# Kernel tuning notes

Hardware: AMD Instinct MI355X
Metric: run time of the kernel (lower is better)

## Reference

```python
import jax, jax.numpy as jnp
import numpy as np

B, S, F, K = 64, 1024, 128, 64  # batch, seq(=l), feat(=d), bottleneck k


def setup_inputs() -> dict:
    key = jax.random.key(0)
    ks = jax.random.split(key, 24)
    r = lambda k_, sh, s=0.05: (jax.random.normal(k_, sh, dtype=jnp.float32) * s)
    inp = {
        'f1_norm': jax.random.normal(ks[0], (B, S, F), dtype=jnp.float32),
        'f2_norm': jax.random.normal(ks[1], (B, S, F), dtype=jnp.float32),
        'f3_norm': jax.random.normal(ks[2], (B, S, F), dtype=jnp.float32),
        # AMLP params (Linear(F, 2F))
        'Wi': r(ks[3], (2 * F, F)), 'bi': r(ks[4], (2 * F,)),
        'Wq': r(ks[5], (2 * F, F)), 'bq': r(ks[6], (2 * F,)),
        'Wvp': r(ks[7], (2 * F, F)), 'bvp': r(ks[8], (2 * F,)),
        # affine_{a,v,l}: Linear(l, l, bias=False) -> weight [l, l]
        'Aa': r(ks[9], (S, S)), 'Av': r(ks[10], (S, S)), 'Al': r(ks[11], (S, S)),
        # W_{a,v,t}: Linear(l, k) -> [k, l]
        'Wa': r(ks[12], (K, S)), 'Wv': r(ks[13], (K, S)), 'Wt': r(ks[14], (K, S)),
        # W_c{a,v,t}: Linear(2d, k) -> [k, 2F]
        'Wca': r(ks[15], (K, 2 * F)), 'Wcv': r(ks[16], (K, 2 * F)), 'Wct': r(ks[17], (K, 2 * F)),
        # W_h{a,v,t}: Linear(k, l) -> [l, k]
        'Wha': r(ks[18], (S, K)), 'Whv': r(ks[19], (S, K)), 'Wht': r(ks[20], (S, K)),
    }
    return inp


def _amlp(txt, aud, vis, Wi, bi, Wq, bq, Wvp, bvp):
    f1 = jnp.einsum('bsf,gf->bsg', txt, Wi) + bi  # [B,S,2F]
    f2 = jnp.einsum('bsf,gf->bsg', aud, Wq) + bq
    f3 = jnp.einsum('bsf,gf->bsg', vis, Wvp) + bvp
    n1 = jnp.linalg.norm(f1)
    n2 = jnp.linalg.norm(f2)
    n3 = jnp.linalg.norm(f3)
    # faithful to source: third term is scalar factor3 * norm3 (broadcast)
    exp_out = (n1 / (n1 + n2)) * f1 + (n2 / (n1 + n2)) * f2 + (n3 / (n1 + n2 + n3)) * n3
    b, s, g = exp_out.shape
    z = exp_out.reshape(b, s, g // 2, 2).sum(-1)  # AvgPool1d(2,2) * 2 == pair sum
    # F.normalize default dim=1 (over sequence axis for 3D tensor)
    z = z / jnp.maximum(jnp.linalg.norm(z, axis=1, keepdims=True), 1e-12)
    return z  # [B,S,F]


def reference(f1_norm, f2_norm, f3_norm, Wi, bi, Wq, bq, Wvp, bvp,
              Aa, Av, Al, Wa, Wv, Wt, Wca, Wcv, Wct, Wha, Whv, Wht):
    txt, aud, vis = f1_norm, f2_norm, f3_norm
    G = _amlp(txt, aud, vis, Wi, bi, Wq, bq, Wvp, bvp)  # [B,S,F]

    G_ag = jnp.concatenate([aud, G], axis=-1)  # [B,S,2F]
    G_vg = jnp.concatenate([vis, G], axis=-1)
    G_lg = jnp.concatenate([txt, G], axis=-1)
    scale = np.sqrt(G_ag.shape[-1]).astype(np.float32)  # sqrt(2F); same for all three

    # a_j = affine(G_xg^T); att = x^T @ a_j^T  ==  x^T @ (A @ G_xg)
    AGa = jnp.einsum('ts,bsc->btc', Aa, G_ag)
    C_a = jnp.tanh(jnp.einsum('bsf,bsc->bfc', aud, AGa) / scale)  # [B,F,2F]
    AGv = jnp.einsum('ts,bsc->btc', Av, G_ag)  # NOTE: source bug uses G_ag, not G_vg
    C_v = jnp.tanh(jnp.einsum('bsf,bsc->bfc', vis, AGv) / scale)
    AGl = jnp.einsum('ts,bsc->btc', Al, G_lg)
    C_t = jnp.tanh(jnp.einsum('bsf,bsc->bfc', txt, AGl) / scale)

    H_a = jax.nn.relu(jnp.einsum('bfc,kc->bfk', C_a, Wca) + jnp.einsum('bsf,ks->bfk', aud, Wa))
    H_v = jax.nn.relu(jnp.einsum('bfc,kc->bfk', C_v, Wcv) + jnp.einsum('bsf,ks->bfk', vis, Wv))
    H_t = jax.nn.relu(jnp.einsum('bfc,kc->bfk', C_t, Wct) + jnp.einsum('bsf,ks->bfk', txt, Wt))

    out_a = jnp.einsum('bfk,sk->bsf', H_a, Wha) + aud  # [B,S,F]
    out_v = jnp.einsum('bfk,sk->bsf', H_v, Whv) + vis
    out_t = jnp.einsum('bfk,sk->bsf', H_t, Wht) + txt
    return (out_t, out_a, out_v)
```

## Files before the change

kernel.cpp:

```cpp
#include <hip/hip_runtime.h>
#include <math.h>

constexpr int Bb = 64;
constexpr int Ss = 1024;
constexpr int Ff = 128;
constexpr int G2 = 256;
constexpr int Kk = 64;
constexpr int NA = 1024;

typedef __bf16 bfrag __attribute__((ext_vector_type(8)));
typedef float  facc  __attribute__((ext_vector_type(4)));
typedef short  s8v   __attribute__((ext_vector_type(8)));
typedef short  s4v   __attribute__((ext_vector_type(4)));

__device__ __forceinline__ short f2bfs(float f) {
  union { float f; unsigned u; } v; v.f = f;
  unsigned r = v.u + 0x7FFFu + ((v.u >> 16) & 1u);
  return (short)(r >> 16);
}
__device__ __forceinline__ float bf2fs(short s) {
  union { unsigned u; float f; } v; v.u = ((unsigned)(unsigned short)s) << 16;
  return v.f;
}
__device__ __forceinline__ facc mfma16(bfrag a, bfrag b, facc c) {
  return __builtin_amdgcn_mfma_f32_16x16x32_bf16(a, b, c, 0, 0, 0);
}
__device__ __forceinline__ void gld16(const void* g, void* l) {
  __builtin_amdgcn_global_load_lds(
      (const __attribute__((address_space(1))) void*)g,
      (__attribute__((address_space(3))) void*)l, 16, 0, 0);
}

__global__ void k_transpose(const float* __restrict__ aud, const float* __restrict__ vis,
                            const float* __restrict__ txt, short* __restrict__ xT) {
  __shared__ float tile[64][65];
  int z = blockIdx.z;
  int mod = z >> 6, b = z & 63;
  const float* x = (mod == 0) ? aud : (mod == 1) ? vis : txt;
  int s0 = blockIdx.x * 64, f0 = blockIdx.y * 64;
  int tid = threadIdx.x;
  {
    int fg = tid & 15, sb = tid >> 4;
#pragma unroll
    for (int i = 0; i < 4; ++i) {
      int si = i * 16 + sb;
      float4 v = *(const float4*)(x + ((size_t)b * Ss + s0 + si) * Ff + f0 + fg * 4);
      tile[si][fg * 4 + 0] = v.x;
      tile[si][fg * 4 + 1] = v.y;
      tile[si][fg * 4 + 2] = v.z;
      tile[si][fg * 4 + 3] = v.w;
    }
  }
  __syncthreads();
  short* dst = xT + ((size_t)mod * Bb + b) * Ff * Ss;
  {
    int sg = tid & 15, fb = tid >> 4;
#pragma unroll
    for (int i = 0; i < 4; ++i) {
      int fi = i * 16 + fb;
      s4v v;
      v[0] = f2bfs(tile[sg * 4 + 0][fi]);
      v[1] = f2bfs(tile[sg * 4 + 1][fi]);
      v[2] = f2bfs(tile[sg * 4 + 2][fi]);
      v[3] = f2bfs(tile[sg * 4 + 3][fi]);
      *(s4v*)(dst + (size_t)(f0 + fi) * Ss + s0 + sg * 4) = v;
    }
  }
}

__global__ void k_build_aextT(const float* __restrict__ Aa, const float* __restrict__ Av,
                              const float* __restrict__ Al, short* __restrict__ aextT) {
  __shared__ float tile[64][65];
  int mod = blockIdx.z;
  const float* A = (mod == 0) ? Aa : (mod == 1) ? Av : Al;
  short* dst = aextT + (size_t)mod * NA * Ss;
  int n0 = blockIdx.x * 64, t0 = blockIdx.y * 64;
  int tid = threadIdx.x;
  {
    int fg = tid & 15, sb = tid >> 4;
#pragma unroll
    for (int i = 0; i < 4; ++i) {
      int ti = i * 16 + sb;
      float4 v = *(const float4*)(A + (size_t)(t0 + ti) * Ss + n0 + fg * 4);
      tile[ti][fg * 4 + 0] = v.x;
      tile[ti][fg * 4 + 1] = v.y;
      tile[ti][fg * 4 + 2] = v.z;
      tile[ti][fg * 4 + 3] = v.w;
    }
  }
  __syncthreads();
  {
    int tg = tid & 15, nb = tid >> 4;
#pragma unroll
    for (int i = 0; i < 4; ++i) {
      int nj = i * 16 + nb;
      s4v v;
      v[0] = f2bfs(tile[tg * 4 + 0][nj]);
      v[1] = f2bfs(tile[tg * 4 + 1][nj]);
      v[2] = f2bfs(tile[tg * 4 + 2][nj]);
      v[3] = f2bfs(tile[tg * 4 + 3][nj]);
      *(s4v*)(dst + (size_t)(n0 + nj) * Ss + t0 + tg * 4) = v;
    }
  }
}

__global__ void k_build_w(const float* __restrict__ Wca, const float* __restrict__ Wcv,
                          const float* __restrict__ Wct, const float* __restrict__ Wha,
                          const float* __restrict__ Whv, const float* __restrict__ Wht,
                          const float* __restrict__ Wi, const float* __restrict__ Wq,
                          const float* __restrict__ Wvp, const float* __restrict__ Wa,
                          const float* __restrict__ Wv, const float* __restrict__ Wt,
                          short* __restrict__ wcb, short* __restrict__ whb,
                          short* __restrict__ wbar, short* __restrict__ wsb) {
  int idx = blockIdx.x * 256 + threadIdx.x;
  const int n1 = 3 * Kk * G2;
  const int n2 = n1 + 3 * Ss * Kk;
  const int n3 = n2 + 3 * G2 * Ff;
  if (idx < n1) {
    int mod = idx / (Kk * G2), r = idx - mod * (Kk * G2);
    const float* W = (mod == 0) ? Wca : (mod == 1) ? Wcv : Wct;
    wcb[idx] = f2bfs(W[r]);
  } else if (idx < n2) {
    int j = idx - n1;
    int mod = j / (Ss * Kk), r = j - mod * (Ss * Kk);
    const float* W = (mod == 0) ? Wha : (mod == 1) ? Whv : Wht;
    whb[j] = f2bfs(W[r]);
  } else if (idx < n3) {
    int j = idx - n2;
    int mod = j / (G2 * Ff), r = j - mod * (G2 * Ff);
    int n = r >> 7, k = r & 127;
    int t = n >> 4, nl = n & 15;
    int c = k >> 5, q = (k >> 3) & 3, e = k & 7;
    const float* W = (mod == 0) ? Wi : (mod == 1) ? Wq : Wvp;
    wbar[mod * G2 * Ff + (((t * 4 + c) * 64 + q * 16 + nl) * 8) + e] = f2bfs(W[r]);
  } else {
    int j = idx - n3;
    int mod = j / (Kk * Ss), r = j - mod * (Kk * Ss);
    const float* W = (mod == 0) ? Wa : (mod == 1) ? Wv : Wt;
    wsb[j] = f2bfs(W[r]);
  }
}

__global__ void __launch_bounds__(256, 3) k_amlp(
    const float* __restrict__ txt, const float* __restrict__ aud, const float* __restrict__ vis,
    const float* __restrict__ bi, const float* __restrict__ bq, const float* __restrict__ bvp,
    const short* __restrict__ wbar,
    short* __restrict__ p1, short* __restrict__ p2, float* __restrict__ sumsq) {
  int mod = blockIdx.y;
  const float* x    = (mod == 0) ? txt : (mod == 1) ? aud : vis;
  const float* bias = (mod == 0) ? bi  : (mod == 1) ? bq  : bvp;
  const short* wbm  = wbar + mod * G2 * Ff;
  short* pout = (mod == 0) ? p1 : (mod == 1) ? p2 : nullptr;

  __shared__ float wred[4];
  int tid = threadIdx.x, lane = tid & 63, wave = tid >> 6;
  int quad = lane >> 4, nl = lane & 15;

  bfrag wreg[4][4];
#pragma unroll
  for (int tt = 0; tt < 4; ++tt)
#pragma unroll
    for (int c = 0; c < 4; ++c)
      wreg[tt][c] = *(const bfrag*)(wbm + ((((wave * 4 + tt) * 4 + c) * 64 + lane) * 8));

  float bia[4];
#pragma unroll
  for (int tt = 0; tt < 4; ++tt) bia[tt] = bias[wave * 64 + tt * 16 + nl];

  const float* xblk = x + (size_t)(blockIdx.x * 256) * Ff;
  facc zero = {0.f, 0.f, 0.f, 0.f};
  float sq = 0.f;

  float4 buf[8];
  {
    const float* xrow = xblk + (size_t)nl * Ff;
#pragma unroll
    for (int c = 0; c < 4; ++c) {
      buf[c * 2]     = *(const float4*)(xrow + c * 32 + quad * 8);
      buf[c * 2 + 1] = *(const float4*)(xrow + c * 32 + quad * 8 + 4);
    }
  }

  for (int g = 0; g < 16; ++g) {
    bfrag af[4];
#pragma unroll
    for (int c = 0; c < 4; ++c) {
      float4 a0 = buf[c * 2], a1 = buf[c * 2 + 1];
      af[c][0] = (__bf16)a0.x; af[c][1] = (__bf16)a0.y;
      af[c][2] = (__bf16)a0.z; af[c][3] = (__bf16)a0.w;
      af[c][4] = (__bf16)a1.x; af[c][5] = (__bf16)a1.y;
      af[c][6] = (__bf16)a1.z; af[c][7] = (__bf16)a1.w;
    }
    if (g < 15) {
      const float* xrow = xblk + (size_t)((g + 1) * 16 + nl) * Ff;
#pragma unroll
      for (int c = 0; c < 4; ++c) {
        buf[c * 2]     = *(const float4*)(xrow + c * 32 + quad * 8);
        buf[c * 2 + 1] = *(const float4*)(xrow + c * 32 + quad * 8 + 4);
      }
    }
    facc acc[4];
#pragma unroll
    for (int tt = 0; tt < 4; ++tt) acc[tt] = zero;
#pragma unroll
    for (int c = 0; c < 4; ++c)
#pragma unroll
      for (int tt = 0; tt < 4; ++tt)
        acc[tt] = mfma16(af[c], wreg[tt][c], acc[tt]);

    int drow = blockIdx.x * 256 + g * 16 + quad * 4;
#pragma unroll
    for (int tt = 0; tt < 4; ++tt)
#pragma unroll
      for (int r = 0; r < 4; ++r) {
        float fv = acc[tt][r] + bia[tt];
        sq += fv * fv;
        if (pout) {
          float fo = fv + __shfl_xor(fv, 1, 64);
          if ((lane & 1) == 0)
            pout[(size_t)(drow + r) * Ff + wave * 32 + tt * 8 + (nl >> 1)] = f2bfs(fo);
        }
      }
  }
  for (int off = 32; off > 0; off >>= 1) sq += __shfl_down(sq, off, 64);
  if (lane == 0) wred[wave] = sq;
  __syncthreads();
  if (tid == 0) atomicAdd(&sumsq[mod], wred[0] + wred[1] + wred[2] + wred[3]);
}

__global__ void k_colnorm(const short* __restrict__ p1, const short* __restrict__ p2,
                          const float* __restrict__ sumsq, float* __restrict__ colnsq) {
  __shared__ float part[16][128];
  float n1 = sqrtf(sumsq[0]), n2 = sqrtf(sumsq[1]), n3 = sqrtf(sumsq[2]);
  float w1 = n1 / (n1 + n2), w2 = n2 / (n1 + n2);
  float tc = 2.f * n3 * n3 / (n1 + n2 + n3);
  int b = blockIdx.x, s0 = blockIdx.y * 128;
  int tid = threadIdx.x, fi = (tid & 15) * 8, sl = tid >> 4;
  float a[8];
#pragma unroll
  for (int j = 0; j < 8; ++j) a[j] = 0.f;
  for (int st = 0; st < 8; ++st) {
    size_t off = ((size_t)b * Ss + s0 + st * 16 + sl) * Ff + fi;
    s8v v1 = *(const s8v*)(p1 + off);
    s8v v2 = *(const s8v*)(p2 + off);
#pragma unroll
    for (int j = 0; j < 8; ++j) {
      float z = w1 * bf2fs(v1[j]) + w2 * bf2fs(v2[j]) + tc;
      a[j] += z * z;
    }
  }
#pragma unroll
  for (int j = 0; j < 8; ++j) part[sl][fi + j] = a[j];
  __syncthreads();
  if (tid < 128) {
    float s = 0.f;
    for (int i = 0; i < 16; ++i) s += part[i][tid];
    atomicAdd(&colnsq[b * Ff + tid], s);
  }
}

__global__ void k_gnormT(const short* __restrict__ p1, const short* __restrict__ p2,
                         const float* __restrict__ sumsq, const float* __restrict__ colnsq,
                         short* __restrict__ gT) {
  __shared__ float tile[64][65];
  __shared__ float invcn[64];
  float n1 = sqrtf(sumsq[0]), n2 = sqrtf(sumsq[1]), n3 = sqrtf(sumsq[2]);
  float w1 = n1 / (n1 + n2), w2 = n2 / (n1 + n2);
  float tc = 2.f * n3 * n3 / (n1 + n2 + n3);
  int b = blockIdx.z, s0 = blockIdx.x * 64, f0 = blockIdx.y * 64;
  int tid = threadIdx.x;
  if (tid < 64)
    invcn[tid] = 1.f / fmaxf(sqrtf(colnsq[b * Ff + f0 + tid]), 1e-12f);
  __syncthreads();
  for (int i = 0; i < 16; ++i) {
    int idx = i * 256 + tid;
    int si = idx >> 6, fi = idx & 63;
    size_t off = ((size_t)b * Ss + s0 + si) * Ff + f0 + fi;
    float z = w1 * bf2fs(p1[off]) + w2 * bf2fs(p2[off]) + tc;
    tile[si][fi] = z * invcn[fi];
  }
  __syncthreads();
  short* dst = gT + (size_t)b * Ff * Ss;
  {
    int sg = tid & 15, fb = tid >> 4;
#pragma unroll
    for (int i = 0; i < 4; ++i) {
      int fi = i * 16 + fb;
      s4v v;
      v[0] = f2bfs(tile[sg * 4 + 0][fi]);
      v[1] = f2bfs(tile[sg * 4 + 1][fi]);
      v[2] = f2bfs(tile[sg * 4 + 2][fi]);
      v[3] = f2bfs(tile[sg * 4 + 3][fi]);
      *(s4v*)(dst + (size_t)(f0 + fi) * Ss + s0 + sg * 4) = v;
    }
  }
}

__global__ void __launch_bounds__(256) k_mgemm(const short* __restrict__ xT,
                                               const short* __restrict__ aextT,
                                               short* __restrict__ mx) {
  int mod = blockIdx.z;
  const short* Ap = xT + (size_t)mod * Bb * Ff * Ss;
  const short* Bp = aextT + (size_t)mod * NA * Ss;
  short* Op = mx + (size_t)mod * Bb * Ff * NA;
  int bx = blockIdx.x;
  int swzx = (bx & 7) * 8 + (bx >> 3);
  int M0 = swzx * 128, N0 = blockIdx.y * 128;
  __shared__ short As[128 * 64];
  __shared__ short Bs[128 * 64];
  int tid = threadIdx.x, lane = tid & 63, wave = tid >> 6;
  int quad = lane >> 4, nl = lane & 15;
  int wm = (wave >> 1) * 64, wn = (wave & 1) * 64;
  facc zero = {0.f, 0.f, 0.f, 0.f};
  facc acc[4][4];
  for (int i = 0; i < 4; ++i) for (int j = 0; j < 4; ++j) acc[i][j] = zero;
  for (int k0 = 0; k0 < Ss; k0 += 64) {
    __syncthreads();
#pragma unroll
    for (int i = 0; i < 4; ++i) {
      int idx = i * 256 + tid;
      int r = idx >> 3, cs = ((idx & 7) ^ (r & 7)) * 8;
      gld16(Ap + (size_t)(M0 + r) * Ss + k0 + cs, As + idx * 8);
      gld16(Bp + (size_t)(N0 + r) * Ss + k0 + cs, Bs + idx * 8);
    }
    __syncthreads();
#pragma unroll
    for (int kc = 0; kc < 2; ++kc) {
      bfrag a[4], bfr[4];
      for (int mt = 0; mt < 4; ++mt) {
        int row = wm + mt * 16 + nl;
        a[mt] = *(const bfrag*)(As + row * 64 + (((kc * 4 + quad) ^ (row & 7)) * 8));
      }
      for (int nt = 0; nt < 4; ++nt) {
        int row = wn + nt * 16 + nl;
        bfr[nt] = *(const bfrag*)(Bs + row * 64 + (((kc * 4 + quad) ^ (row & 7)) * 8));
      }
      for (int mt = 0; mt < 4; ++mt)
        for (int nt = 0; nt < 4; ++nt)
          acc[mt][nt] = mfma16(a[mt], bfr[nt], acc[mt][nt]);
    }
  }
  for (int mt = 0; mt < 4; ++mt)
    for (int nt = 0; nt < 4; ++nt)
      for (int r = 0; r < 4; ++r) {
        int row = M0 + wm + mt * 16 + quad * 4 + r;
        int col = N0 + wn + nt * 16 + nl;
        Op[(size_t)row * NA + col] = f2bfs(acc[mt][nt][r]);
      }
}

__global__ void __launch_bounds__(256) k_chgemm(const short* __restrict__ mx,
                                                const short* __restrict__ xT,
                                                const short* __restrict__ gT,
                                                const short* __restrict__ wcb,
                                                const short* __restrict__ wsb,
                                                short* __restrict__ h) {
  int b = blockIdx.x, mod = blockIdx.y, half = blockIdx.z;
  int r0 = half * 64;
  const short* Ap = mx + ((size_t)mod * Bb + b) * Ff * NA;
  const short* xTb = xT + (size_t)((mod == 2) ? 2 : 0) * Bb * Ff * Ss + (size_t)b * Ff * Ss;
  const short* xTm = xT + (size_t)mod * Bb * Ff * Ss + (size_t)b * Ff * Ss;
  const short* gTb = gT + (size_t)b * Ff * Ss;
  const short* Wp  = wcb + (size_t)mod * Kk * G2;
  const short* Wsp = wsb + (size_t)mod * Kk * Ss;
  short* Hp = h + ((size_t)mod * Bb + b) * Ff * Kk;

  __shared__ short smem[64 * 272 + 64 * 72];
  short* As = smem;
  short* Bs = smem + 64 * 64;

  int tid = threadIdx.x, lane = tid & 63, wave = tid >> 6;
  int quad = lane >> 4, nl = lane & 15;
  int wn = wave * 64;
  facc zero = {0.f, 0.f, 0.f, 0.f};
  facc acc[4][4];
  facc t2a[4];
  for (int i = 0; i < 4; ++i) for (int j = 0; j < 4; ++j) acc[i][j] = zero;
  for (int i = 0; i < 4; ++i) t2a[i] = zero;
  for (int k0 = 0; k0 < Ss; k0 += 64) {
    __syncthreads();
#pragma unroll
    for (int i = 0; i < 2; ++i) {
      int idx = i * 256 + tid;
      int r = idx >> 3, cs = ((idx & 7) ^ (r & 7)) * 8;
      gld16(Ap + (size_t)(r0 + r) * NA + k0 + cs, As + idx * 8);
    }
#pragma unroll
    for (int i = 0; i < 8; ++i) {
      int idx = i * 256 + tid;
      int r = idx >> 3, cs = ((idx & 7) ^ (r & 7)) * 8;
      const short* src = (r < 128) ? (xTb + (size_t)r * Ss) : (gTb + (size_t)(r - 128) * Ss);
      gld16(src + k0 + cs, Bs + idx * 8);
    }
    __syncthreads();
#pragma unroll
    for (int kc = 0; kc < 2; ++kc) {
      bfrag a[4], bfr[4], xa[4], wf;
      for (int mt = 0; mt < 4; ++mt) {
        int row = mt * 16 + nl;
        a[mt] = *(const bfrag*)(As + row * 64 + (((kc * 4 + quad) ^ (row & 7)) * 8));
      }
      for (int nt = 0; nt < 4; ++nt) {
        int row = wn + nt * 16 + nl;
        bfr[nt] = *(const bfrag*)(Bs + row * 64 + (((kc * 4 + quad) ^ (row & 7)) * 8));
      }
      for (int mt = 0; mt < 4; ++mt)
        xa[mt] = *(const bfrag*)(xTm + (size_t)(r0 + mt * 16 + nl) * Ss + k0 + kc * 32 + quad * 8);
      wf = *(const bfrag*)(Wsp + (size_t)(wave * 16 + nl) * Ss + k0 + kc * 32 + quad * 8);
      for (int mt = 0; mt < 4; ++mt)
        for (int nt = 0; nt < 4; ++nt)
          acc[mt][nt] = mfma16(a[mt], bfr[nt], acc[mt][nt]);
      for (int mt = 0; mt < 4; ++mt)
        t2a[mt] = mfma16(xa[mt], wf, t2a[mt]);
    }
  }
  __syncthreads();
  short* Cs  = smem;
  short* T2s = smem + 64 * 272;
  for (int mt = 0; mt < 4; ++mt)
    for (int nt = 0; nt < 4; ++nt)
      for (int r = 0; r < 4; ++r) {
        int row = mt * 16 + quad * 4 + r;
        int col = wn + nt * 16 + nl;
        Cs[row * 272 + col] = f2bfs(tanhf(acc[mt][nt][r] * 0.0625f));
      }
  for (int mt = 0; mt < 4; ++mt)
    for (int r = 0; r < 4; ++r)
      T2s[(mt * 16 + quad * 4 + r) * 72 + wave * 16 + nl] = f2bfs(t2a[mt][r]);
  __syncthreads();
  facc hacc[4];
  for (int nt = 0; nt < 4; ++nt) hacc[nt] = zero;
  for (int k0 = 0; k0 < G2; k0 += 32) {
    bfrag ca = *(const bfrag*)(Cs + (wave * 16 + nl) * 272 + k0 + quad * 8);
    for (int nt = 0; nt < 4; ++nt) {
      bfrag wb = *(const bfrag*)(Wp + (size_t)(nt * 16 + nl) * G2 + k0 + quad * 8);
      hacc[nt] = mfma16(ca, wb, hacc[nt]);
    }
  }
  for (int nt = 0; nt < 4; ++nt)
    for (int r = 0; r < 4; ++r) {
      int lrow = wave * 16 + quad * 4 + r;
      int col = nt * 16 + nl;
      float v = hacc[nt][r] + bf2fs(T2s[lrow * 72 + col]);
      Hp[(size_t)(r0 + lrow) * Kk + col] = f2bfs(fmaxf(v, 0.f));
    }
}

__global__ void k_outgemm(const short* __restrict__ whb, const short* __restrict__ h,
                          const float* __restrict__ txt, const float* __restrict__ aud,
                          const float* __restrict__ vis, float* __restrict__ outp) {
  int s0 = blockIdx.x * 128, b = blockIdx.y, mod = blockIdx.z;
  const short* Wp = whb + (size_t)mod * Ss * Kk;
  const short* Hp = h + ((size_t)mod * Bb + b) * Ff * Kk;
  const float* xres = ((mod == 0) ? aud : (mod == 1) ? vis : txt) + (size_t)b * Ss * Ff;
  int slot = (mod == 0) ? 1 : (mod == 1) ? 2 : 0;
  float* Op = outp + ((size_t)slot * Bb + b) * Ss * Ff;
  int tid = threadIdx.x, lane = tid & 63, wave = tid >> 6;
  int quad = lane >> 4, nl = lane & 15;
  int wm = (wave >> 1) * 64, wn = (wave & 1) * 64;
  facc zero = {0.f, 0.f, 0.f, 0.f};
  facc acc[4][4];
  for (int i = 0; i < 4; ++i) for (int j = 0; j < 4; ++j) acc[i][j] = zero;
  for (int k0 = 0; k0 < Kk; k0 += 32) {
    bfrag a[4], bfr[4];
    for (int mt = 0; mt < 4; ++mt)
      a[mt] = *(const bfrag*)(Wp + (size_t)(s0 + wm + mt * 16 + nl) * Kk + k0 + quad * 8);
    for (int nt = 0; nt < 4; ++nt)
      bfr[nt] = *(const bfrag*)(Hp + (size_t)(wn + nt * 16 + nl) * Kk + k0 + quad * 8);
    for (int mt = 0; mt < 4; ++mt)
      for (int nt = 0; nt < 4; ++nt)
        acc[mt][nt] = mfma16(a[mt], bfr[nt], acc[mt][nt]);
  }
  for (int mt = 0; mt < 4; ++mt)
    for (int nt = 0; nt < 4; ++nt)
      for (int r = 0; r < 4; ++r) {
        int srow = s0 + wm + mt * 16 + quad * 4 + r;
        int col = wn + nt * 16 + nl;
        size_t o = (size_t)srow * Ff + col;
        Op[o] = acc[mt][nt][r] + xres[o];
      }
}

extern "C" void kernel_launch(void* const* d_in, const int* in_sizes, int n_in,
                              void* d_out, int out_size, void* d_ws, size_t ws_size,
                              hipStream_t stream) {
  const float* txt = (const float*)d_in[0];
  const float* aud = (const float*)d_in[1];
  const float* vis = (const float*)d_in[2];
  const float* Wi  = (const float*)d_in[3];
  const float* bi  = (const float*)d_in[4];
  const float* Wq  = (const float*)d_in[5];
  const float* bq  = (const float*)d_in[6];
  const float* Wvp = (const float*)d_in[7];
  const float* bvp = (const float*)d_in[8];
  const float* Aa  = (const float*)d_in[9];
  const float* Av  = (const float*)d_in[10];
  const float* Al  = (const float*)d_in[11];
  const float* Wa  = (const float*)d_in[12];
  const float* Wv  = (const float*)d_in[13];
  const float* Wt  = (const float*)d_in[14];
  const float* Wca = (const float*)d_in[15];
  const float* Wcv = (const float*)d_in[16];
  const float* Wct = (const float*)d_in[17];
  const float* Wha = (const float*)d_in[18];
  const float* Whv = (const float*)d_in[19];
  const float* Wht = (const float*)d_in[20];

  char* w = (char*)d_ws;
  float* sumsq  = (float*)w;
  float* colnsq = (float*)(w + 256);
  size_t off = 65536;
  short* xT    = (short*)(w + off); off += (size_t)3 * Bb * Ff * Ss * 2;
  short* aextT = (short*)(w + off); off += (size_t)3 * NA * Ss * 2;
  short* gT    = (short*)(w + off); off += (size_t)Bb * Ff * Ss * 2;
  short* mx    = (short*)(w + off);
  short* p1    = mx;
  short* p2    = mx + (size_t)Bb * Ss * Ff;
  off += (size_t)3 * Bb * Ff * NA * 2;
  short* h     = (short*)(w + off); off += (size_t)3 * Bb * Ff * Kk * 2;
  short* wcb   = (short*)(w + off); off += (size_t)3 * Kk * G2 * 2;
  short* whb   = (short*)(w + off); off += (size_t)3 * Ss * Kk * 2;
  short* wbar  = (short*)(w + off); off += (size_t)3 * G2 * Ff * 2;
  short* wsb   = (short*)(w + off); off += (size_t)3 * Kk * Ss * 2;

  hipMemsetAsync(d_ws, 0, 65536, stream);
  k_transpose<<<dim3(16, 2, 192), 256, 0, stream>>>(aud, vis, txt, xT);
  k_build_aextT<<<dim3(16, 16, 3), 256, 0, stream>>>(Aa, Av, Al, aextT);
  k_build_w<<<(3 * Kk * G2 + 3 * Ss * Kk + 3 * G2 * Ff + 3 * Kk * Ss) / 256, 256, 0, stream>>>(
      Wca, Wcv, Wct, Wha, Whv, Wht, Wi, Wq, Wvp, Wa, Wv, Wt, wcb, whb, wbar, wsb);
  k_amlp<<<dim3(Bb * Ss / 256, 3), 256, 0, stream>>>(txt, aud, vis, bi, bq, bvp,
                                                     wbar, p1, p2, sumsq);
  k_colnorm<<<dim3(Bb, 8), 256, 0, stream>>>(p1, p2, sumsq, colnsq);
  k_gnormT<<<dim3(16, 2, Bb), 256, 0, stream>>>(p1, p2, sumsq, colnsq, gT);
  k_mgemm<<<dim3(Bb * Ff / 128, NA / 128, 3), 256, 0, stream>>>(xT, aextT, mx);
  k_chgemm<<<dim3(Bb, 3, 2), 256, 0, stream>>>(mx, xT, gT, wcb, wsb, h);
  k_outgemm<<<dim3(Ss / 128, Bb, 3), 256, 0, stream>>>(whb, h, txt, aud, vis, (float*)d_out);
}
```

Before: 466.3 us.

## Move x·Ws bottleneck GEMM from chgemm into extra mgemm blocks

The x^T·W_s term used by H is now computed in a separate slice of k_mgemm blocks (grid y index 8), one block per batch and modality. The result goes to a new workspace buffer t2. k_chgemm no longer issues per-iteration global loads of x and W_s or the extra MFMAs, and only reads t2 in its epilogue. The intent is to shorten the inner loop of the low-occupancy chgemm kernel by moving that work to a kernel with more parallel blocks. In exchange there is a small extra round trip through global memory, and the added blocks load operands directly from global memory without staging in LDS.

After: 466.0 us. No clear change (-0.1%).

```diff
diff --git a/kernel.cpp b/kernel.cpp
--- a/kernel.cpp
+++ b/kernel.cpp
@@ -298,20 +298,49 @@
 
 __global__ void __launch_bounds__(256) k_mgemm(const short* __restrict__ xT,
                                                const short* __restrict__ aextT,
-                                               short* __restrict__ mx) {
+                                               const short* __restrict__ wsb,
+                                               short* __restrict__ mx,
+                                               short* __restrict__ t2) {
   int mod = blockIdx.z;
+  int bx = blockIdx.x;
+  int swzx = (bx & 7) * 8 + (bx >> 3);
+  int tid = threadIdx.x, lane = tid & 63, wave = tid >> 6;
+  int quad = lane >> 4, nl = lane & 15;
+  facc zero = {0.f, 0.f, 0.f, 0.f};
+
+  if (blockIdx.y == 8) {
+    int b = swzx;
+    const short* xTm = xT + ((size_t)mod * Bb + b) * Ff * Ss;
+    const short* Wsp = wsb + (size_t)mod * Kk * Ss;
+    short* t2p = t2 + ((size_t)mod * Bb + b) * Ff * Kk;
+    int wm = wave * 32;
+    facc acc[2][4];
+    for (int i = 0; i < 2; ++i) for (int j = 0; j < 4; ++j) acc[i][j] = zero;
+    for (int k0 = 0; k0 < Ss; k0 += 32) {
+      bfrag a[2], bfr[4];
+      for (int mt = 0; mt < 2; ++mt)
+        a[mt] = *(const bfrag*)(xTm + (size_t)(wm + mt * 16 + nl) * Ss + k0 + quad * 8);
+      for (int nt = 0; nt < 4; ++nt)
+        bfr[nt] = *(const bfrag*)(Wsp + (size_t)(nt * 16 + nl) * Ss + k0 + quad * 8);
+      for (int mt = 0; mt < 2; ++mt)
+        for (int nt = 0; nt < 4; ++nt)
+          acc[mt][nt] = mfma16(a[mt], bfr[nt], acc[mt][nt]);
+    }
+    for (int mt = 0; mt < 2; ++mt)
+      for (int nt = 0; nt < 4; ++nt)
+        for (int r = 0; r < 4; ++r)
+          t2p[(size_t)(wm + mt * 16 + quad * 4 + r) * Kk + nt * 16 + nl] =
+              f2bfs(acc[mt][nt][r]);
+    return;
+  }
+
   const short* Ap = xT + (size_t)mod * Bb * Ff * Ss;
   const short* Bp = aextT + (size_t)mod * NA * Ss;
   short* Op = mx + (size_t)mod * Bb * Ff * NA;
-  int bx = blockIdx.x;
-  int swzx = (bx & 7) * 8 + (bx >> 3);
   int M0 = swzx * 128, N0 = blockIdx.y * 128;
   __shared__ short As[128 * 64];
   __shared__ short Bs[128 * 64];
-  int tid = threadIdx.x, lane = tid & 63, wave = tid >> 6;
-  int quad = lane >> 4, nl = lane & 15;
   int wm = (wave >> 1) * 64, wn = (wave & 1) * 64;
-  facc zero = {0.f, 0.f, 0.f, 0.f};
   facc acc[4][4];
   for (int i = 0; i < 4; ++i) for (int j = 0; j < 4; ++j) acc[i][j] = zero;
   for (int k0 = 0; k0 < Ss; k0 += 64) {
@@ -353,19 +382,18 @@
                                                 const short* __restrict__ xT,
                                                 const short* __restrict__ gT,
                                                 const short* __restrict__ wcb,
-                                                const short* __restrict__ wsb,
+                                                const short* __restrict__ t2,
                                                 short* __restrict__ h) {
   int b = blockIdx.x, mod = blockIdx.y, half = blockIdx.z;
   int r0 = half * 64;
   const short* Ap = mx + ((size_t)mod * Bb + b) * Ff * NA;
   const short* xTb = xT + (size_t)((mod == 2) ? 2 : 0) * Bb * Ff * Ss + (size_t)b * Ff * Ss;
-  const short* xTm = xT + (size_t)mod * Bb * Ff * Ss + (size_t)b * Ff * Ss;
   const short* gTb = gT + (size_t)b * Ff * Ss;
-  const short* Wp  = wcb + (size_t)mod * Kk * G2;
-  const short* Wsp = wsb + (size_t)mod * Kk * Ss;
+  const short* Wp = wcb + (size_t)mod * Kk * G2;
+  const short* T2p = t2 + ((size_t)mod * Bb + b) * Ff * Kk;
   short* Hp = h + ((size_t)mod * Bb + b) * Ff * Kk;
 
-  __shared__ short smem[64 * 272 + 64 * 72];
+  __shared__ short smem[64 * 64 + 256 * 64];
   short* As = smem;
   short* Bs = smem + 64 * 64;
 
@@ -374,9 +402,7 @@
   int wn = wave * 64;
   facc zero = {0.f, 0.f, 0.f, 0.f};
   facc acc[4][4];
-  facc t2a[4];
   for (int i = 0; i < 4; ++i) for (int j = 0; j < 4; ++j) acc[i][j] = zero;
-  for (int i = 0; i < 4; ++i) t2a[i] = zero;
   for (int k0 = 0; k0 < Ss; k0 += 64) {
     __syncthreads();
 #pragma unroll
@@ -395,7 +421,7 @@
     __syncthreads();
 #pragma unroll
     for (int kc = 0; kc < 2; ++kc) {
-      bfrag a[4], bfr[4], xa[4], wf;
+      bfrag a[4], bfr[4];
       for (int mt = 0; mt < 4; ++mt) {
         int row = mt * 16 + nl;
         a[mt] = *(const bfrag*)(As + row * 64 + (((kc * 4 + quad) ^ (row & 7)) * 8));
@@ -405,33 +431,24 @@
         bfr[nt] = *(const bfrag*)(Bs + row * 64 + (((kc * 4 + quad) ^ (row & 7)) * 8));
       }
       for (int mt = 0; mt < 4; ++mt)
-        xa[mt] = *(const bfrag*)(xTm + (size_t)(r0 + mt * 16 + nl) * Ss + k0 + kc * 32 + quad * 8);
-      wf = *(const bfrag*)(Wsp + (size_t)(wave * 16 + nl) * Ss + k0 + kc * 32 + quad * 8);
-      for (int mt = 0; mt < 4; ++mt)
         for (int nt = 0; nt < 4; ++nt)
           acc[mt][nt] = mfma16(a[mt], bfr[nt], acc[mt][nt]);
-      for (int mt = 0; mt < 4; ++mt)
-        t2a[mt] = mfma16(xa[mt], wf, t2a[mt]);
-    }
-  }
-  __syncthreads();
-  short* Cs  = smem;
-  short* T2s = smem + 64 * 272;
+    }
+  }
+  __syncthreads();
+  short* Cs = smem;
   for (int mt = 0; mt < 4; ++mt)
     for (int nt = 0; nt < 4; ++nt)
       for (int r = 0; r < 4; ++r) {
         int row = mt * 16 + quad * 4 + r;
         int col = wn + nt * 16 + nl;
-        Cs[row * 272 + col] = f2bfs(tanhf(acc[mt][nt][r] * 0.0625f));
-      }
-  for (int mt = 0; mt < 4; ++mt)
-    for (int r = 0; r < 4; ++r)
-      T2s[(mt * 16 + quad * 4 + r) * 72 + wave * 16 + nl] = f2bfs(t2a[mt][r]);
+        Cs[row * 280 + col] = f2bfs(tanhf(acc[mt][nt][r] * 0.0625f));
+      }
   __syncthreads();
   facc hacc[4];
   for (int nt = 0; nt < 4; ++nt) hacc[nt] = zero;
   for (int k0 = 0; k0 < G2; k0 += 32) {
-    bfrag ca = *(const bfrag*)(Cs + (wave * 16 + nl) * 272 + k0 + quad * 8);
+    bfrag ca = *(const bfrag*)(Cs + (wave * 16 + nl) * 280 + k0 + quad * 8);
     for (int nt = 0; nt < 4; ++nt) {
       bfrag wb = *(const bfrag*)(Wp + (size_t)(nt * 16 + nl) * G2 + k0 + quad * 8);
       hacc[nt] = mfma16(ca, wb, hacc[nt]);
@@ -441,7 +458,7 @@
     for (int r = 0; r < 4; ++r) {
       int lrow = wave * 16 + quad * 4 + r;
       int col = nt * 16 + nl;
-      float v = hacc[nt][r] + bf2fs(T2s[lrow * 72 + col]);
+      float v = hacc[nt][r] + bf2fs(T2p[(size_t)(r0 + lrow) * Kk + col]);
       Hp[(size_t)(r0 + lrow) * Kk + col] = f2bfs(fmaxf(v, 0.f));
     }
 }
@@ -522,6 +539,7 @@
   short* whb   = (short*)(w + off); off += (size_t)3 * Ss * Kk * 2;
   short* wbar  = (short*)(w + off); off += (size_t)3 * G2 * Ff * 2;
   short* wsb   = (short*)(w + off); off += (size_t)3 * Kk * Ss * 2;
+  short* t2    = (short*)(w + off); off += (size_t)3 * Bb * Ff * Kk * 2;
 
   hipMemsetAsync(d_ws, 0, 65536, stream);
   k_transpose<<<dim3(16, 2, 192), 256, 0, stream>>>(aud, vis, txt, xT);
@@ -532,7 +550,7 @@
                                                      wbar, p1, p2, sumsq);
   k_colnorm<<<dim3(Bb, 8), 256, 0, stream>>>(p1, p2, sumsq, colnsq);
   k_gnormT<<<dim3(16, 2, Bb), 256, 0, stream>>>(p1, p2, sumsq, colnsq, gT);
-  k_mgemm<<<dim3(Bb * Ff / 128, NA / 128, 3), 256, 0, stream>>>(xT, aextT, mx);
-  k_chgemm<<<dim3(Bb, 3, 2), 256, 0, stream>>>(mx, xT, gT, wcb, wsb, h);
+  k_mgemm<<<dim3(Bb * Ff / 128, 9, 3), 256, 0, stream>>>(xT, aextT, wsb, mx, t2);
+  k_chgemm<<<dim3(Bb, 3, 2), 256, 0, stream>>>(mx, xT, gT, wcb, t2, h);
   k_outgemm<<<dim3(Ss / 128, Bb, 3), 256, 0, stream>>>(whb, h, txt, aud, vis, (float*)d_out);
 }
```
